# Optimization experiments

Hardware: AMD Instinct MI355X
Metric: run time of the kernel (lower is better)

## Reference

```python
import jax, jax.numpy as jnp
import numpy as np
from jax.scipy.linalg import expm

DIM = 1024
N_ROT = 3


def setup_inputs() -> dict:
    key = jax.random.key(0)
    k1, k2 = jax.random.split(key)
    x = jax.random.normal(k1, (4, 4096, DIM), dtype=jnp.float32)
    # raw parameter tensors; skew-symmetrization (as in reset_parameters) done in reference
    generators = jax.random.normal(k2, (N_ROT, DIM, DIM), dtype=jnp.float32) * 0.02
    return {"x": x, "generators": generators}


def reference(x, generators):
    # skew-symmetrize each generator: G <- 0.5*(G - G^T)
    gens = 0.5 * (generators - jnp.swapaxes(generators, -1, -2))
    # sequential rotations: x = x @ expm(G_i) for each of the N_ROT generators
    for i in range(N_ROT):
        rot = expm(gens[i])  # [DIM, DIM] orthogonal rotation
        x = x @ rot
    return x
```

## Files before the change

### kernel.cpp

```cpp
#include <hip/hip_runtime.h>

#define S 1048576
typedef unsigned short u16;
typedef unsigned int u32;
typedef __attribute__((ext_vector_type(8))) short s8v;
typedef __attribute__((ext_vector_type(4))) float f4v;

__device__ __forceinline__ float bf2f(u16 u){
    union { float f; u32 u; } v; v.u = ((u32)u) << 16; return v.f;
}
__device__ __forceinline__ u16 f2bf(float x){
    u32 u = __float_as_uint(x);
    u32 r = (u + 0x7FFFu + ((u >> 16) & 1u)) >> 16;
    return (u16)r;
}
__device__ __forceinline__ void splitf(float x, u16& h, u16& l){
    h = f2bf(x);
    l = f2bf(x - bf2f(h));
}
__device__ __forceinline__ float pairf(const u16* H, const u16* L, size_t off){
    return bf2f(H[off]) + bf2f(L[off]);
}
__device__ __forceinline__ int sidx(int r, int c){ return (r<<6) + (((c) ^ (r&7))<<3); }
__device__ __forceinline__ void gl16(const void* g, void* l){
    __builtin_amdgcn_global_load_lds((const __attribute__((address_space(1))) void*)g,
                                     (__attribute__((address_space(3))) void*)l, 16, 0, 0);
}
__device__ __forceinline__ void xconv1(const float* __restrict__ X, u16* __restrict__ Xh, int u, int t){
    const size_t idx8 = (size_t)u*2048 + (size_t)t*8;
    float4 v0 = *(const float4*)(X+idx8);
    float4 v1 = *(const float4*)(X+idx8+4);
    float xs[8] = {v0.x,v0.y,v0.z,v0.w,v1.x,v1.y,v1.z,v1.w};
    s8v h;
    #pragma unroll
    for (int i = 0; i < 8; ++i) h[i] = (short)f2bf(xs[i]);
    *(s8v*)(Xh+idx8) = h;
}

__global__ __launch_bounds__(256) void pre_k(const float* __restrict__ G, u16* __restrict__ Abase,
                                             const float* __restrict__ X, u16* __restrict__ Xh){
    __shared__ float Gt[64][65];
    const int bid = blockIdx.x;
    const int t = threadIdx.x;
    if (bid >= 768){
        for (int u = bid - 768; u < 2731; u += 1024) xconv1(X, Xh, u, t);
        return;
    }
    const int bx = bid & 15, by = (bid >> 4) & 15, z = bid >> 8;
    const float* Gz = G + (size_t)z*S;
    u16* Ah = Abase + (size_t)z*2*S;
    u16* Al = Ah + S;
    const int row = t >> 2, cq = (t & 3) << 4;
    const int r0 = by << 6, c0 = bx << 6;
    #pragma unroll
    for (int g = 0; g < 4; ++g){
        float4 v = *(const float4*)(Gz + (size_t)(c0+row)*1024 + r0 + cq + g*4);
        Gt[row][cq+g*4+0]=v.x; Gt[row][cq+g*4+1]=v.y; Gt[row][cq+g*4+2]=v.z; Gt[row][cq+g*4+3]=v.w;
    }
    __syncthreads();
    #pragma unroll
    for (int g = 0; g < 2; ++g){
        const float* p = Gz + (size_t)(r0+row)*1024 + c0 + cq + g*8;
        float4 v0 = *(const float4*)(p);
        float4 v1 = *(const float4*)(p+4);
        float xs[8] = {v0.x,v0.y,v0.z,v0.w,v1.x,v1.y,v1.z,v1.w};
        s8v sh, sl;
        #pragma unroll
        for (int i = 0; i < 8; ++i){
            float gt = Gt[cq + g*8 + i][row];
            u16 h,l; splitf(0.5f*(xs[i]-gt), h, l);
            sh[i] = (short)h; sl[i] = (short)l;
        }
        *(s8v*)(Ah + (size_t)(r0+row)*1024 + c0 + cq + g*8) = sh;
        *(s8v*)(Al + (size_t)(r0+row)*1024 + c0 + cq + g*8) = sl;
    }
}

template<int MODE, bool XFUSE>
__global__ __launch_bounds__(256) void gemm64_k(const u16* __restrict__ Abase, const u16* __restrict__ Btbase,
                                                u16* __restrict__ Cbase,
                                                const u16* __restrict__ Pab, const u16* __restrict__ Pa2b,
                                                u16* __restrict__ O2base, u16* __restrict__ E2t,
                                                const float* __restrict__ X, u16* __restrict__ Xh,
                                                int u0, int u1){
    __shared__ u16 lds[3*8192];
    const int t = threadIdx.x;
    if (XFUSE && blockIdx.x >= 16){
        const int nb = (int)gridDim.x - 16;
        const int e = ((int)(blockIdx.z*gridDim.y + blockIdx.y))*nb + ((int)blockIdx.x - 16);
        const int E = nb*(int)gridDim.y*(int)gridDim.z;
        for (int u = u0 + e; u < u1; u += E) xconv1(X, Xh, u, t);
        return;
    }
    const int z = blockIdx.z;
    int bx, by;
    if (XFUSE){ bx = blockIdx.x; by = blockIdx.y; }
    else {
        const int lin = (int)blockIdx.x + ((int)blockIdx.y << 4);
        const int sw = (lin & 7)*32 + (lin >> 3);
        bx = sw & 15; by = sw >> 4;
    }
    const u16* Ah = Abase  + (size_t)z*2*S;
    const u16* Bh = Btbase + (size_t)z*2*S; const u16* Bl = Bh + S;
    u16* Ch = Cbase + (size_t)z*2*S;
    const u16* Pah = Pab + (size_t)z*2*S;   const u16* Pal = Pah + S;
    const u16* P2h = Pa2b + (size_t)z*2*S;
    u16* O2h = O2base + (size_t)z*2*S;
    const int brow = by << 6, bcol = bx << 6;
    const int lane = t & 63, w = t >> 6;
    const int wm = (w >> 1) << 5, wn = (w & 1) << 5;
    const int lr = lane & 15, g = lane >> 4;
    int qq[2]; size_t goA[2], goB[2];
    #pragma unroll
    for (int i = 0; i < 2; ++i){
        int q = (((w<<1)+i)<<6) + lane;
        int r = q >> 3, c = lane & 7;
        qq[i] = q << 3;
        goA[i] = (size_t)(brow+r)*1024 + ((c^(r&7))<<3);
        goB[i] = (size_t)(bcol+r)*1024 + ((c^(r&7))<<3);
    }
    auto issue = [&](int kt){
        u16* L = lds + (kt % 3) * 8192;
        const int k0 = kt << 6;
        #pragma unroll
        for (int i = 0; i < 2; ++i){
            gl16(Ah + goA[i] + k0, L + qq[i]);
            gl16(Bh + goB[i] + k0, L + 4096 + qq[i]);
        }
    };
    issue(0); issue(1);
    f4v acc[2][2] = {};
    for (int kt = 0; kt < 16; ++kt){
        if (kt < 15) asm volatile("s_waitcnt vmcnt(4)" ::: "memory");
        else         asm volatile("s_waitcnt vmcnt(0)" ::: "memory");
        __builtin_amdgcn_s_barrier();
        __builtin_amdgcn_sched_barrier(0);
        if (kt < 14) issue(kt + 2);
        const u16* L = lds + (kt % 3) * 8192;
        #pragma unroll
        for (int ks = 0; ks < 2; ++ks){
            const int ch = (ks << 2) + g;
            s8v a_h[2], b_h[2];
            #pragma unroll
            for (int f = 0; f < 2; ++f){
                const int ra = wm+(f<<4)+lr, rb = wn+(f<<4)+lr;
                a_h[f] = *(const s8v*)&L[sidx(ra,ch)];
                b_h[f] = *(const s8v*)&L[4096 + sidx(rb,ch)];
            }
            __builtin_amdgcn_s_setprio(1);
            #pragma unroll
            for (int mf = 0; mf < 2; ++mf)
                #pragma unroll
                for (int nf = 0; nf < 2; ++nf)
                    acc[mf][nf] = __builtin_amdgcn_mfma_f32_16x16x32_bf16(a_h[mf], b_h[nf], acc[mf][nf], 0,0,0);
            __builtin_amdgcn_s_setprio(0);
        }
    }
    const int orr = g << 2;
    #pragma unroll
    for (int mf = 0; mf < 2; ++mf)
        #pragma unroll
        for (int nf = 0; nf < 2; ++nf)
            #pragma unroll
            for (int r = 0; r < 4; ++r){
                const int orow = brow + wm + (mf<<4) + orr + r;
                const int ocol = bcol + wn + (nf<<4) + lr;
                const size_t off = (size_t)orow*1024 + ocol;
                const float av = acc[mf][nf][r];
                if (MODE == 0){
                    Ch[off] = f2bf(av);
                }
                if (MODE == 1){
                    Ch[off] = f2bf(av);
                    float a = pairf(Bh, Bl, off);
                    O2h[off] = f2bf((1.0f/6.0f)*a - (1.0f/24.0f)*av);
                }
                if (MODE == 2){
                    float a  = pairf(Pah, Pal, off);
                    float a2 = bf2f(P2h[off]);
                    float e = a - 0.5f*a2 - av + (orow == ocol ? 1.0f : 0.0f);
                    u16 h = f2bf(e);
                    O2h[off] = h;
                    if (z == 2) E2t[(size_t)ocol*1024 + orow] = h;
                }
            }
}

__global__ __launch_bounds__(512) void gemm_big3(const u16* __restrict__ Xh, const u16* __restrict__ Rth,
                                                 float* __restrict__ Y){
    __shared__ u16 lds[2][32768];
    const int bid = blockIdx.x;
    const int swz = (bid & 7)*32 + (bid >> 3);
    const int by = swz >> 2, bx = swz & 3;
    const int brow = by << 8, bcol = bx << 8;
    const int t = threadIdx.x;
    const int lane = t & 63, w = t >> 6;
    const int wm = (w >> 2) << 7, wn = (w & 3) << 6;
    const int lr = lane & 15, g = lane >> 4;
    int xq[4]; size_t gx[4], gb[4];
    #pragma unroll
    for (int i = 0; i < 4; ++i){
        int q = (((w<<2)+i)<<6) + lane;
        int r = q >> 3, c = lane & 7;
        xq[i] = q << 3;
        gx[i] = (size_t)(brow+r)*1024 + ((c^(r&7))<<3);
        gb[i] = (size_t)(bcol+r)*1024 + ((c^(r&7))<<3);
    }
    f4v acc[8][4] = {};
    {
        u16* L = lds[0];
        #pragma unroll
        for (int i = 0; i < 4; ++i){
            gl16(Xh  + gx[i], L + xq[i]);
            gl16(Rth + gb[i], L + 16384 + xq[i]);
        }
    }
    int cur = 0;
    for (int kt = 0; kt < 16; ++kt){
        __syncthreads();
        if (kt < 15){
            u16* L = lds[cur^1];
            const int k0 = (kt+1) << 6;
            #pragma unroll
            for (int i = 0; i < 4; ++i){
                gl16(Xh  + gx[i] + k0, L + xq[i]);
                gl16(Rth + gb[i] + k0, L + 16384 + xq[i]);
            }
        }
        const u16* L = lds[cur];
        #pragma unroll
        for (int ks = 0; ks < 2; ++ks){
            const int ch = (ks << 2) + g;
            s8v bh[4];
            #pragma unroll
            for (int nf = 0; nf < 4; ++nf){
                const int rb = wn+(nf<<4)+lr;
                bh[nf] = *(const s8v*)&L[16384 + sidx(rb,ch)];
            }
            __builtin_amdgcn_s_setprio(1);
            #pragma unroll
            for (int mf = 0; mf < 8; ++mf){
                const int ra = wm+(mf<<4)+lr;
                s8v a = *(const s8v*)&L[sidx(ra,ch)];
                #pragma unroll
                for (int nf = 0; nf < 4; ++nf)
                    acc[mf][nf] = __builtin_amdgcn_mfma_f32_16x16x32_bf16(a, bh[nf], acc[mf][nf], 0,0,0);
            }
            __builtin_amdgcn_s_setprio(0);
        }
        cur ^= 1;
    }
    const int orr = g << 2;
    #pragma unroll
    for (int mf = 0; mf < 8; ++mf)
        #pragma unroll
        for (int nf = 0; nf < 4; ++nf)
            #pragma unroll
            for (int r = 0; r < 4; ++r){
                int orow = brow + wm + (mf<<4) + orr + r;
                int ocol = bcol + wn + (nf<<4) + lr;
                Y[(size_t)orow*1024 + ocol] = acc[mf][nf][r];
            }
}

__global__ __launch_bounds__(256) void gemm_big_f(const float* __restrict__ Xv, const u16* __restrict__ Rth,
                                                  float* __restrict__ Y){
    __shared__ u16 Xs[128*64], Bhs[128*64];
    const int bid = blockIdx.x;
    const int swz = (bid & 7)*128 + (bid >> 3);
    const int bx = swz & 7, by = swz >> 3;
    const int brow = by << 7, bcol = bx << 7;
    const int t = threadIdx.x;
    const int sr = t >> 1, cb = (t & 1) << 2;
    const int lane = t & 63, w = t >> 6;
    const int wm = (w >> 1) << 6, wn = (w & 1) << 6;
    const int lr = lane & 15, g = lane >> 4;
    s8v xr[4], bhr[4];
    auto load_tile = [&](int k0){
        #pragma unroll
        for (int i = 0; i < 4; ++i){
            const size_t bo = (size_t)(bcol+sr)*1024 + k0 + ((cb+i)<<3);
            bhr[i] = *(const s8v*)(Rth + bo);
        }
        #pragma unroll
        for (int i = 0; i < 4; ++i){
            const float* p = Xv + (size_t)(brow+sr)*1024 + k0 + ((cb+i)<<3);
            float4 f0 = *(const float4*)(p), f1 = *(const float4*)(p+4);
            float xs[8] = {f0.x,f0.y,f0.z,f0.w,f1.x,f1.y,f1.z,f1.w};
            #pragma unroll
            for (int j = 0; j < 8; ++j) xr[i][j] = (short)f2bf(xs[j]);
        }
    };
    load_tile(0);
    f4v acc[4][4] = {};
    for (int k0 = 0; k0 < 1024; k0 += 64){
        __syncthreads();
        #pragma unroll
        for (int i = 0; i < 4; ++i){
            const int si = sidx(sr, cb+i);
            *(s8v*)&Xs[si]  = xr[i];
            *(s8v*)&Bhs[si] = bhr[i];
        }
        __syncthreads();
        if (k0 < 960) load_tile(k0 + 64);
        #pragma unroll
        for (int ks = 0; ks < 2; ++ks){
            const int ch = (ks << 2) + g;
            s8v bhf[4];
            #pragma unroll
            for (int nf = 0; nf < 4; ++nf)
                bhf[nf] = *(const s8v*)&Bhs[sidx(wn+(nf<<4)+lr, ch)];
            #pragma unroll
            for (int mf = 0; mf < 4; ++mf){
                s8v ah = *(const s8v*)&Xs[sidx(wm+(mf<<4)+lr, ch)];
                #pragma unroll
                for (int nf = 0; nf < 4; ++nf)
                    acc[mf][nf] = __builtin_amdgcn_mfma_f32_16x16x32_bf16(ah, bhf[nf], acc[mf][nf], 0,0,0);
            }
        }
    }
    const int orr = g << 2;
    #pragma unroll
    for (int mf = 0; mf < 4; ++mf)
        #pragma unroll
        for (int nf = 0; nf < 4; ++nf)
            #pragma unroll
            for (int r = 0; r < 4; ++r){
                int orow = brow + wm + (mf<<4) + orr + r;
                int ocol = bcol + wn + (nf<<4) + lr;
                Y[(size_t)orow*1024 + ocol] = acc[mf][nf][r];
            }
}

extern "C" void kernel_launch(void* const* d_in, const int* in_sizes, int n_in,
                              void* d_out, int out_size, void* d_ws, size_t ws_size,
                              hipStream_t stream) {
    const float* X = (const float*)d_in[0];
    const float* G = (const float*)d_in[1];
    float* out = (float*)d_out;
    u16* ob = (u16*)d_out;
    auto slot = [&](int i){ return ob + (size_t)i*2*S; };
    u16* RT = (u16*)d_ws;
    u16* Xh = RT + (size_t)2*S;
    const bool ws_ok = ws_size >= (size_t)36*S;

    dim3 b(256);
    pre_k<<<dim3(ws_ok ? 1792 : 768), b, 0, stream>>>(G, slot(0), X, Xh);
    gemm64_k<1,false><<<dim3(16,16,3), b, 0, stream>>>(slot(0), slot(0), slot(3),
                                                       slot(0), slot(0), slot(6), slot(15),
                                                       X, Xh, 0, 0);
    gemm64_k<2,false><<<dim3(16,16,3), b, 0, stream>>>(slot(6), slot(3), slot(14),
                                                       slot(0), slot(3), slot(9), slot(15),
                                                       X, Xh, 0, 0);
    if (ws_ok){
        gemm64_k<0,true><<<dim3(64,16,1), b, 0, stream>>>(slot(15), slot(10), slot(12),
                                                          slot(0), slot(0), slot(12), slot(15),
                                                          X, Xh, 2731, 5462);
        gemm64_k<0,true><<<dim3(64,16,1), b, 0, stream>>>(slot(12), slot(9), RT,
                                                          slot(0), slot(0), RT, slot(15),
                                                          X, Xh, 5462, 8192);
        gemm_big3<<<dim3(256), dim3(512), 0, stream>>>(Xh, RT, out);
    } else {
        gemm64_k<0,false><<<dim3(16,16,1), b, 0, stream>>>(slot(15), slot(10), slot(12),
                                                           slot(0), slot(0), slot(12), slot(15),
                                                           X, Xh, 0, 0);
        gemm64_k<0,false><<<dim3(16,16,1), b, 0, stream>>>(slot(12), slot(9), RT,
                                                           slot(0), slot(0), RT, slot(15),
                                                           X, Xh, 0, 0);
        gemm_big_f<<<dim3(1024), b, 0, stream>>>(X, RT, out);
    }
}
```

Measured before the change: 115.4 us.

## Restructure big GEMM main loop into four-phase ping-pong with split A/B prefetch

The main 16384x1024x1024 bf16 GEMM loop is reorganized into four quadrant phases per K-tile. Each phase loads a subset of A/B fragments into registers, then issues a barrier-separated MFMA cluster at raised priority. Global prefetches for the next tile are split so A is issued at the start and B midway, spreading memory traffic across the compute phases. The intent is to interleave LDS reads, global loads and MFMA across waves so they overlap better. The cost is many more barriers and manual waitcnt/sched_barrier control, which could serialize waves or cause stalls if the schedule does not line up.

```diff
diff --git a/kernel.cpp b/kernel.cpp
--- a/kernel.cpp
+++ b/kernel.cpp
@@ -186,9 +186,9 @@
             }
 }
 
-__global__ __launch_bounds__(512) void gemm_big3(const u16* __restrict__ Xh, const u16* __restrict__ Rth,
+__global__ __launch_bounds__(512) void gemm_big8(const u16* __restrict__ Xh, const u16* __restrict__ Rth,
                                                  float* __restrict__ Y){
-    __shared__ u16 lds[2][32768];
+    __shared__ u16 lds[2*32768];
     const int bid = blockIdx.x;
     const int swz = (bid & 7)*32 + (bid >> 3);
     const int by = swz >> 2, bx = swz & 3;
@@ -206,49 +206,97 @@
         gx[i] = (size_t)(brow+r)*1024 + ((c^(r&7))<<3);
         gb[i] = (size_t)(bcol+r)*1024 + ((c^(r&7))<<3);
     }
+    auto issueA = [&](int kt){
+        u16* L = lds + ((kt & 1) << 15);
+        const int k0 = kt << 6;
+        #pragma unroll
+        for (int i = 0; i < 4; ++i) gl16(Xh + gx[i] + k0, L + xq[i]);
+    };
+    auto issueB = [&](int kt){
+        u16* L = lds + ((kt & 1) << 15);
+        const int k0 = kt << 6;
+        #pragma unroll
+        for (int i = 0; i < 4; ++i) gl16(Rth + gb[i] + k0, L + 16384 + xq[i]);
+    };
     f4v acc[8][4] = {};
-    {
-        u16* L = lds[0];
-        #pragma unroll
-        for (int i = 0; i < 4; ++i){
-            gl16(Xh  + gx[i], L + xq[i]);
-            gl16(Rth + gb[i], L + 16384 + xq[i]);
-        }
-    }
-    int cur = 0;
+    s8v a[4][2], b[4][2];
+    issueA(0); issueB(0);
+    asm volatile("s_waitcnt vmcnt(0)" ::: "memory");
+    __builtin_amdgcn_s_barrier();
     for (int kt = 0; kt < 16; ++kt){
-        __syncthreads();
-        if (kt < 15){
-            u16* L = lds[cur^1];
-            const int k0 = (kt+1) << 6;
-            #pragma unroll
-            for (int i = 0; i < 4; ++i){
-                gl16(Xh  + gx[i] + k0, L + xq[i]);
-                gl16(Rth + gb[i] + k0, L + 16384 + xq[i]);
-            }
-        }
-        const u16* L = lds[cur];
+        const u16* L = lds + ((kt & 1) << 15);
+        if (kt < 15) issueA(kt + 1);
         #pragma unroll
         for (int ks = 0; ks < 2; ++ks){
             const int ch = (ks << 2) + g;
-            s8v bh[4];
-            #pragma unroll
-            for (int nf = 0; nf < 4; ++nf){
-                const int rb = wn+(nf<<4)+lr;
-                bh[nf] = *(const s8v*)&L[16384 + sidx(rb,ch)];
-            }
-            __builtin_amdgcn_s_setprio(1);
-            #pragma unroll
-            for (int mf = 0; mf < 8; ++mf){
-                const int ra = wm+(mf<<4)+lr;
-                s8v a = *(const s8v*)&L[sidx(ra,ch)];
-                #pragma unroll
-                for (int nf = 0; nf < 4; ++nf)
-                    acc[mf][nf] = __builtin_amdgcn_mfma_f32_16x16x32_bf16(a, bh[nf], acc[mf][nf], 0,0,0);
-            }
-            __builtin_amdgcn_s_setprio(0);
-        }
-        cur ^= 1;
+            #pragma unroll
+            for (int mf = 0; mf < 4; ++mf) a[mf][ks] = *(const s8v*)&L[sidx(wm+(mf<<4)+lr, ch)];
+            #pragma unroll
+            for (int nf = 0; nf < 2; ++nf) b[nf][ks] = *(const s8v*)&L[16384 + sidx(wn+(nf<<4)+lr, ch)];
+        }
+        __builtin_amdgcn_s_barrier();
+        asm volatile("s_waitcnt lgkmcnt(0)" ::: "memory");
+        __builtin_amdgcn_sched_barrier(0);
+        __builtin_amdgcn_s_setprio(1);
+        #pragma unroll
+        for (int mf = 0; mf < 4; ++mf)
+            #pragma unroll
+            for (int nf = 0; nf < 2; ++nf)
+                #pragma unroll
+                for (int ks = 0; ks < 2; ++ks)
+                    acc[mf][nf] = __builtin_amdgcn_mfma_f32_16x16x32_bf16(a[mf][ks], b[nf][ks], acc[mf][nf], 0,0,0);
+        __builtin_amdgcn_s_setprio(0);
+        __builtin_amdgcn_s_barrier();
+        if (kt < 15) issueB(kt + 1);
+        #pragma unroll
+        for (int ks = 0; ks < 2; ++ks){
+            const int ch = (ks << 2) + g;
+            #pragma unroll
+            for (int nf = 2; nf < 4; ++nf) b[nf][ks] = *(const s8v*)&L[16384 + sidx(wn+(nf<<4)+lr, ch)];
+        }
+        __builtin_amdgcn_s_barrier();
+        asm volatile("s_waitcnt lgkmcnt(0)" ::: "memory");
+        __builtin_amdgcn_sched_barrier(0);
+        __builtin_amdgcn_s_setprio(1);
+        #pragma unroll
+        for (int mf = 0; mf < 4; ++mf)
+            #pragma unroll
+            for (int nf = 2; nf < 4; ++nf)
+                #pragma unroll
+                for (int ks = 0; ks < 2; ++ks)
+                    acc[mf][nf] = __builtin_amdgcn_mfma_f32_16x16x32_bf16(a[mf][ks], b[nf][ks], acc[mf][nf], 0,0,0);
+        __builtin_amdgcn_s_setprio(0);
+        __builtin_amdgcn_s_barrier();
+        #pragma unroll
+        for (int ks = 0; ks < 2; ++ks){
+            const int ch = (ks << 2) + g;
+            #pragma unroll
+            for (int mf = 0; mf < 4; ++mf) a[mf][ks] = *(const s8v*)&L[sidx(wm+64+(mf<<4)+lr, ch)];
+        }
+        __builtin_amdgcn_s_barrier();
+        asm volatile("s_waitcnt lgkmcnt(0)" ::: "memory");
+        __builtin_amdgcn_sched_barrier(0);
+        __builtin_amdgcn_s_setprio(1);
+        #pragma unroll
+        for (int mf = 0; mf < 4; ++mf)
+            #pragma unroll
+            for (int nf = 2; nf < 4; ++nf)
+                #pragma unroll
+                for (int ks = 0; ks < 2; ++ks)
+                    acc[4+mf][nf] = __builtin_amdgcn_mfma_f32_16x16x32_bf16(a[mf][ks], b[nf][ks], acc[4+mf][nf], 0,0,0);
+        __builtin_amdgcn_s_setprio(0);
+        __builtin_amdgcn_s_barrier();
+        __builtin_amdgcn_s_setprio(1);
+        #pragma unroll
+        for (int mf = 0; mf < 4; ++mf)
+            #pragma unroll
+            for (int nf = 0; nf < 2; ++nf)
+                #pragma unroll
+                for (int ks = 0; ks < 2; ++ks)
+                    acc[4+mf][nf] = __builtin_amdgcn_mfma_f32_16x16x32_bf16(a[mf][ks], b[nf][ks], acc[4+mf][nf], 0,0,0);
+        __builtin_amdgcn_s_setprio(0);
+        if (kt < 15) asm volatile("s_waitcnt vmcnt(0)" ::: "memory");
+        __builtin_amdgcn_s_barrier();
     }
     const int orr = g << 2;
     #pragma unroll
@@ -359,7 +407,7 @@
         gemm64_k<0,true><<<dim3(64,16,1), b, 0, stream>>>(slot(12), slot(9), RT,
                                                           slot(0), slot(0), RT, slot(15),
                                                           X, Xh, 5462, 8192);
-        gemm_big3<<<dim3(256), dim3(512), 0, stream>>>(Xh, RT, out);
+        gemm_big8<<<dim3(256), dim3(512), 0, stream>>>(Xh, RT, out);
     } else {
         gemm64_k<0,false><<<dim3(16,16,1), b, 0, stream>>>(slot(15), slot(10), slot(12),
                                                            slot(0), slot(0), slot(12), slot(15),
```

Measured after the change: 116.5 us. Within noise of the previous version (+0.9%).

## Fuse X bf16 conversion into big GEMM loads and tile the E2 transpose store

Applied to the files above, without the earlier changes.

The separate X fp32-to-bf16 conversion spread across the prep and small GEMM kernels is removed. The final 256x256-tile GEMM now loads fp32 X directly, converts it in registers and writes it to LDS, while the rotation matrix tile still streams in asynchronously. This drops a full write and re-read of the bf16 X buffer but puts conversion work on the main GEMM's critical path. The transposed E2 store is also staged through LDS so the global writes are coalesced instead of strided.

```diff
diff --git a/kernel.cpp b/kernel.cpp
--- a/kernel.cpp
+++ b/kernel.cpp
@@ -26,26 +26,11 @@
     __builtin_amdgcn_global_load_lds((const __attribute__((address_space(1))) void*)g,
                                      (__attribute__((address_space(3))) void*)l, 16, 0, 0);
 }
-__device__ __forceinline__ void xconv1(const float* __restrict__ X, u16* __restrict__ Xh, int u, int t){
-    const size_t idx8 = (size_t)u*2048 + (size_t)t*8;
-    float4 v0 = *(const float4*)(X+idx8);
-    float4 v1 = *(const float4*)(X+idx8+4);
-    float xs[8] = {v0.x,v0.y,v0.z,v0.w,v1.x,v1.y,v1.z,v1.w};
-    s8v h;
-    #pragma unroll
-    for (int i = 0; i < 8; ++i) h[i] = (short)f2bf(xs[i]);
-    *(s8v*)(Xh+idx8) = h;
-}
-
-__global__ __launch_bounds__(256) void pre_k(const float* __restrict__ G, u16* __restrict__ Abase,
-                                             const float* __restrict__ X, u16* __restrict__ Xh){
+
+__global__ __launch_bounds__(256) void pre_k(const float* __restrict__ G, u16* __restrict__ Abase){
     __shared__ float Gt[64][65];
     const int bid = blockIdx.x;
     const int t = threadIdx.x;
-    if (bid >= 768){
-        for (int u = bid - 768; u < 2731; u += 1024) xconv1(X, Xh, u, t);
-        return;
-    }
     const int bx = bid & 15, by = (bid >> 4) & 15, z = bid >> 8;
     const float* Gz = G + (size_t)z*S;
     u16* Ah = Abase + (size_t)z*2*S;
@@ -76,30 +61,17 @@
     }
 }
 
-template<int MODE, bool XFUSE>
+template<int MODE>
 __global__ __launch_bounds__(256) void gemm64_k(const u16* __restrict__ Abase, const u16* __restrict__ Btbase,
                                                 u16* __restrict__ Cbase,
                                                 const u16* __restrict__ Pab, const u16* __restrict__ Pa2b,
-                                                u16* __restrict__ O2base, u16* __restrict__ E2t,
-                                                const float* __restrict__ X, u16* __restrict__ Xh,
-                                                int u0, int u1){
+                                                u16* __restrict__ O2base, u16* __restrict__ E2t){
     __shared__ u16 lds[3*8192];
     const int t = threadIdx.x;
-    if (XFUSE && blockIdx.x >= 16){
-        const int nb = (int)gridDim.x - 16;
-        const int e = ((int)(blockIdx.z*gridDim.y + blockIdx.y))*nb + ((int)blockIdx.x - 16);
-        const int E = nb*(int)gridDim.y*(int)gridDim.z;
-        for (int u = u0 + e; u < u1; u += E) xconv1(X, Xh, u, t);
-        return;
-    }
     const int z = blockIdx.z;
-    int bx, by;
-    if (XFUSE){ bx = blockIdx.x; by = blockIdx.y; }
-    else {
-        const int lin = (int)blockIdx.x + ((int)blockIdx.y << 4);
-        const int sw = (lin & 7)*32 + (lin >> 3);
-        bx = sw & 15; by = sw >> 4;
-    }
+    const int lin = (int)blockIdx.x + ((int)blockIdx.y << 4);
+    const int sw = (lin & 7)*32 + (lin >> 3);
+    const int bx = sw & 15, by = sw >> 4;
     const u16* Ah = Abase  + (size_t)z*2*S;
     const u16* Bh = Btbase + (size_t)z*2*S; const u16* Bl = Bh + S;
     u16* Ch = Cbase + (size_t)z*2*S;
@@ -157,6 +129,7 @@
         }
     }
     const int orr = g << 2;
+    u16 hsv[2][2][4];
     #pragma unroll
     for (int mf = 0; mf < 2; ++mf)
         #pragma unroll
@@ -181,14 +154,35 @@
                     float e = a - 0.5f*a2 - av + (orow == ocol ? 1.0f : 0.0f);
                     u16 h = f2bf(e);
                     O2h[off] = h;
-                    if (z == 2) E2t[(size_t)ocol*1024 + orow] = h;
-                }
-            }
-}
-
-__global__ __launch_bounds__(512) void gemm_big3(const u16* __restrict__ Xh, const u16* __restrict__ Rth,
-                                                 float* __restrict__ Y){
-    __shared__ u16 lds[2][32768];
+                    hsv[mf][nf][r] = h;
+                }
+            }
+    if (MODE == 2 && z == 2){
+        u16 (*Tt)[72] = (u16(*)[72])lds;
+        __builtin_amdgcn_s_barrier();
+        #pragma unroll
+        for (int mf = 0; mf < 2; ++mf)
+            #pragma unroll
+            for (int nf = 0; nf < 2; ++nf)
+                #pragma unroll
+                for (int r = 0; r < 4; ++r){
+                    const int lrow = wm + (mf<<4) + orr + r;
+                    const int lcol = wn + (nf<<4) + lr;
+                    Tt[lcol][lrow] = hsv[mf][nf][r];
+                }
+        __builtin_amdgcn_s_barrier();
+        const int rr = t >> 2, cc = (t & 3) << 1;
+        #pragma unroll
+        for (int i = 0; i < 2; ++i){
+            s8v v = *(const s8v*)&Tt[rr][(cc+i)<<3];
+            *(s8v*)&E2t[(size_t)(bcol+rr)*1024 + brow + ((cc+i)<<3)] = v;
+        }
+    }
+}
+
+__global__ __launch_bounds__(512) void gemm_big3x(const float* __restrict__ X, const u16* __restrict__ Rth,
+                                                  float* __restrict__ Y){
+    __shared__ u16 lds[2*32768];
     const int bid = blockIdx.x;
     const int swz = (bid & 7)*32 + (bid >> 3);
     const int by = swz >> 2, bx = swz & 3;
@@ -197,37 +191,51 @@
     const int lane = t & 63, w = t >> 6;
     const int wm = (w >> 2) << 7, wn = (w & 3) << 6;
     const int lr = lane & 15, g = lane >> 4;
-    int xq[4]; size_t gx[4], gb[4];
+    int bq[4]; size_t gb[4];
     #pragma unroll
     for (int i = 0; i < 4; ++i){
         int q = (((w<<2)+i)<<6) + lane;
         int r = q >> 3, c = lane & 7;
-        xq[i] = q << 3;
-        gx[i] = (size_t)(brow+r)*1024 + ((c^(r&7))<<3);
+        bq[i] = q << 3;
         gb[i] = (size_t)(bcol+r)*1024 + ((c^(r&7))<<3);
     }
+    int xrow[4], xc[4];
+    #pragma unroll
+    for (int i = 0; i < 4; ++i){ int q = (i<<9) + t; xrow[i] = q >> 3; xc[i] = q & 7; }
+    auto issueB = [&](int kt){
+        u16* L = lds + ((kt & 1) << 15) + 16384;
+        const int k0 = kt << 6;
+        #pragma unroll
+        for (int i = 0; i < 4; ++i) gl16(Rth + gb[i] + k0, L + bq[i]);
+    };
+    float4 xf[4][2];
+    auto loadX = [&](int kt){
+        const int k0 = kt << 6;
+        #pragma unroll
+        for (int i = 0; i < 4; ++i){
+            const float* p = X + (size_t)(brow+xrow[i])*1024 + k0 + (xc[i]<<3);
+            xf[i][0] = *(const float4*)(p);
+            xf[i][1] = *(const float4*)(p+4);
+        }
+    };
+    auto writeX = [&](int kt){
+        u16* L = lds + ((kt & 1) << 15);
+        #pragma unroll
+        for (int i = 0; i < 4; ++i){
+            float xs[8] = {xf[i][0].x, xf[i][0].y, xf[i][0].z, xf[i][0].w,
+                           xf[i][1].x, xf[i][1].y, xf[i][1].z, xf[i][1].w};
+            s8v h;
+            #pragma unroll
+            for (int j = 0; j < 8; ++j) h[j] = (short)f2bf(xs[j]);
+            *(s8v*)&L[sidx(xrow[i], xc[i])] = h;
+        }
+    };
     f4v acc[8][4] = {};
-    {
-        u16* L = lds[0];
-        #pragma unroll
-        for (int i = 0; i < 4; ++i){
-            gl16(Xh  + gx[i], L + xq[i]);
-            gl16(Rth + gb[i], L + 16384 + xq[i]);
-        }
-    }
-    int cur = 0;
+    loadX(0); issueB(0); writeX(0);
     for (int kt = 0; kt < 16; ++kt){
         __syncthreads();
-        if (kt < 15){
-            u16* L = lds[cur^1];
-            const int k0 = (kt+1) << 6;
-            #pragma unroll
-            for (int i = 0; i < 4; ++i){
-                gl16(Xh  + gx[i] + k0, L + xq[i]);
-                gl16(Rth + gb[i] + k0, L + 16384 + xq[i]);
-            }
-        }
-        const u16* L = lds[cur];
+        if (kt < 15){ loadX(kt + 1); issueB(kt + 1); }
+        const u16* L = lds + ((kt & 1) << 15);
         #pragma unroll
         for (int ks = 0; ks < 2; ++ks){
             const int ch = (ks << 2) + g;
@@ -248,80 +256,11 @@
             }
             __builtin_amdgcn_s_setprio(0);
         }
-        cur ^= 1;
+        if (kt < 15) writeX(kt + 1);
     }
     const int orr = g << 2;
     #pragma unroll
     for (int mf = 0; mf < 8; ++mf)
-        #pragma unroll
-        for (int nf = 0; nf < 4; ++nf)
-            #pragma unroll
-            for (int r = 0; r < 4; ++r){
-                int orow = brow + wm + (mf<<4) + orr + r;
-                int ocol = bcol + wn + (nf<<4) + lr;
-                Y[(size_t)orow*1024 + ocol] = acc[mf][nf][r];
-            }
-}
-
-__global__ __launch_bounds__(256) void gemm_big_f(const float* __restrict__ Xv, const u16* __restrict__ Rth,
-                                                  float* __restrict__ Y){
-    __shared__ u16 Xs[128*64], Bhs[128*64];
-    const int bid = blockIdx.x;
-    const int swz = (bid & 7)*128 + (bid >> 3);
-    const int bx = swz & 7, by = swz >> 3;
-    const int brow = by << 7, bcol = bx << 7;
-    const int t = threadIdx.x;
-    const int sr = t >> 1, cb = (t & 1) << 2;
-    const int lane = t & 63, w = t >> 6;
-    const int wm = (w >> 1) << 6, wn = (w & 1) << 6;
-    const int lr = lane & 15, g = lane >> 4;
-    s8v xr[4], bhr[4];
-    auto load_tile = [&](int k0){
-        #pragma unroll
-        for (int i = 0; i < 4; ++i){
-            const size_t bo = (size_t)(bcol+sr)*1024 + k0 + ((cb+i)<<3);
-            bhr[i] = *(const s8v*)(Rth + bo);
-        }
-        #pragma unroll
-        for (int i = 0; i < 4; ++i){
-            const float* p = Xv + (size_t)(brow+sr)*1024 + k0 + ((cb+i)<<3);
-            float4 f0 = *(const float4*)(p), f1 = *(const float4*)(p+4);
-            float xs[8] = {f0.x,f0.y,f0.z,f0.w,f1.x,f1.y,f1.z,f1.w};
-            #pragma unroll
-            for (int j = 0; j < 8; ++j) xr[i][j] = (short)f2bf(xs[j]);
-        }
-    };
-    load_tile(0);
-    f4v acc[4][4] = {};
-    for (int k0 = 0; k0 < 1024; k0 += 64){
-        __syncthreads();
-        #pragma unroll
-        for (int i = 0; i < 4; ++i){
-            const int si = sidx(sr, cb+i);
-            *(s8v*)&Xs[si]  = xr[i];
-            *(s8v*)&Bhs[si] = bhr[i];
-        }
-        __syncthreads();
-        if (k0 < 960) load_tile(k0 + 64);
-        #pragma unroll
-        for (int ks = 0; ks < 2; ++ks){
-            const int ch = (ks << 2) + g;
-            s8v bhf[4];
-            #pragma unroll
-            for (int nf = 0; nf < 4; ++nf)
-                bhf[nf] = *(const s8v*)&Bhs[sidx(wn+(nf<<4)+lr, ch)];
-            #pragma unroll
-            for (int mf = 0; mf < 4; ++mf){
-                s8v ah = *(const s8v*)&Xs[sidx(wm+(mf<<4)+lr, ch)];
-                #pragma unroll
-                for (int nf = 0; nf < 4; ++nf)
-                    acc[mf][nf] = __builtin_amdgcn_mfma_f32_16x16x32_bf16(ah, bhf[nf], acc[mf][nf], 0,0,0);
-            }
-        }
-    }
-    const int orr = g << 2;
-    #pragma unroll
-    for (int mf = 0; mf < 4; ++mf)
         #pragma unroll
         for (int nf = 0; nf < 4; ++nf)
             #pragma unroll
@@ -341,32 +280,16 @@
     u16* ob = (u16*)d_out;
     auto slot = [&](int i){ return ob + (size_t)i*2*S; };
     u16* RT = (u16*)d_ws;
-    u16* Xh = RT + (size_t)2*S;
-    const bool ws_ok = ws_size >= (size_t)36*S;
 
     dim3 b(256);
-    pre_k<<<dim3(ws_ok ? 1792 : 768), b, 0, stream>>>(G, slot(0), X, Xh);
-    gemm64_k<1,false><<<dim3(16,16,3), b, 0, stream>>>(slot(0), slot(0), slot(3),
-                                                       slot(0), slot(0), slot(6), slot(15),
-                                                       X, Xh, 0, 0);
-    gemm64_k<2,false><<<dim3(16,16,3), b, 0, stream>>>(slot(6), slot(3), slot(14),
-                                                       slot(0), slot(3), slot(9), slot(15),
-                                                       X, Xh, 0, 0);
-    if (ws_ok){
-        gemm64_k<0,true><<<dim3(64,16,1), b, 0, stream>>>(slot(15), slot(10), slot(12),
-                                                          slot(0), slot(0), slot(12), slot(15),
-                                                          X, Xh, 2731, 5462);
-        gemm64_k<0,true><<<dim3(64,16,1), b, 0, stream>>>(slot(12), slot(9), RT,
-                                                          slot(0), slot(0), RT, slot(15),
-                                                          X, Xh, 5462, 8192);
-        gemm_big3<<<dim3(256), dim3(512), 0, stream>>>(Xh, RT, out);
-    } else {
-        gemm64_k<0,false><<<dim3(16,16,1), b, 0, stream>>>(slot(15), slot(10), slot(12),
-                                                           slot(0), slot(0), slot(12), slot(15),
-                                                           X, Xh, 0, 0);
-        gemm64_k<0,false><<<dim3(16,16,1), b, 0, stream>>>(slot(12), slot(9), RT,
-                                                           slot(0), slot(0), RT, slot(15),
-                                                           X, Xh, 0, 0);
-        gemm_big_f<<<dim3(1024), b, 0, stream>>>(X, RT, out);
-    }
-}
+    pre_k<<<dim3(768), b, 0, stream>>>(G, slot(0));
+    gemm64_k<1><<<dim3(16,16,3), b, 0, stream>>>(slot(0), slot(0), slot(3),
+                                                 slot(0), slot(0), slot(6), slot(15));
+    gemm64_k<2><<<dim3(16,16,3), b, 0, stream>>>(slot(6), slot(3), slot(14),
+                                                 slot(0), slot(3), slot(9), slot(15));
+    gemm64_k<0><<<dim3(16,16,1), b, 0, stream>>>(slot(15), slot(10), slot(12),
+                                                 slot(0), slot(0), slot(12), slot(15));
+    gemm64_k<0><<<dim3(16,16,1), b, 0, stream>>>(slot(12), slot(9), RT,
+                                                 slot(0), slot(0), RT, slot(15));
+    gemm_big3x<<<dim3(256), dim3(512), 0, stream>>>(X, RT, out);
+}
```

Result: faster. 106.6 us (-7.6%).
